# Performance work log

Measured on AMD Instinct MI355X. Metric: run time of the kernel, lower is better.

## Reference

```python
import jax, jax.numpy as jnp
import numpy as np

B, S, H, E, D = 4, 4096, 1024, 8, 256

def setup_inputs() -> dict:
    key = jax.random.key(0)
    k0, k1, k2, k3, k4 = jax.random.split(key, 5)
    scale_h = 1.0 / np.sqrt(H)
    scale_d = 1.0 / np.sqrt(D)
    return {
        "x": jax.random.normal(k0, (B, S, H), dtype=jnp.float32),
        "gate_w": jax.random.normal(k1, (E, H), dtype=jnp.float32) * scale_h,  # nn.Linear(H,E) weight [E,H]
        "wg": jax.random.normal(k2, (E, H, D), dtype=jnp.float32) * scale_h,   # gate_proj per expert
        "wu": jax.random.normal(k3, (E, H, D), dtype=jnp.float32) * scale_h,   # up_proj per expert
        "wd": jax.random.normal(k4, (E, D, H), dtype=jnp.float32) * scale_d,   # down_proj per expert
    }

def reference(x, gate_w, wg, wu, wd):
    b, s, h = x.shape
    xf = x.reshape(-1, h)                                   # [T, H]
    logits = jnp.einsum('th,eh->te', xf, gate_w)            # router logits
    expert_idx = jnp.argmax(logits, axis=-1)                # top-1 expert per token
    onehot = jax.nn.one_hot(expert_idx, gate_w.shape[0], dtype=x.dtype)  # [T, E]
    g = jnp.einsum('th,ehd->etd', xf, wg)                   # [E, T, D]
    u = jnp.einsum('th,ehd->etd', xf, wu)                   # [E, T, D]
    inter = jnp.square(jax.nn.relu(g)) * u                  # ReLU^2 * up
    inter = inter * onehot.T[:, :, None]                    # zero out non-selected (expert, token) pairs
    out = jnp.einsum('etd,edh->th', inter, wd)              # combine over experts
    return out.reshape(b, s, h)
```

## Files before the change

### kernel.cpp

```cpp
#include <hip/hip_runtime.h>
#include <hip/hip_bf16.h>

#define TOK 16384
#define HD  1024
#define DD  256
#define NE  8

typedef __attribute__((ext_vector_type(8))) short short8;
typedef __attribute__((ext_vector_type(4))) float floatx4;
typedef unsigned short u16;

static __device__ __forceinline__ u16 f2bf(float f) {
  __hip_bfloat16 h = __float2bfloat16(f);
  return *reinterpret_cast<u16*>(&h);
}
static __device__ __forceinline__ short8 cvt8(const float* p) {
  float4 a = *(const float4*)p;
  float4 b = *(const float4*)(p + 4);
  u16 t[8] = {f2bf(a.x), f2bf(a.y), f2bf(a.z), f2bf(a.w),
              f2bf(b.x), f2bf(b.y), f2bf(b.z), f2bf(b.w)};
  return *(short8*)t;
}

__global__ __launch_bounds__(256) void prep_kernel(
    const float* __restrict__ wg, const float* __restrict__ wu,
    const float* __restrict__ wd, const float* __restrict__ x,
    const float* __restrict__ gw,
    u16* __restrict__ wgT, u16* __restrict__ wuT, u16* __restrict__ wdT,
    u16* __restrict__ xbf,
    int* __restrict__ counts, int* __restrict__ tlist)
{
  __shared__ u16 tile[64][72];
  __shared__ int sexp[16];
  __shared__ int sbase[NE];
  int bid = blockIdx.x;
  int tid = threadIdx.x;

  if (bid < 1536) {
    const float* src; u16* dst; int R, C;
    if (bid < 512)       { src = wg; dst = wgT; R = HD; C = DD; }
    else if (bid < 1024) { src = wu; dst = wuT; R = HD; C = DD; bid -= 512; }
    else                 { src = wd; dst = wdT; R = DD; C = HD; bid -= 1024; }
    int e = bid >> 6, t = bid & 63;
    int ntc = C >> 6;
    int tr = t / ntc, tc = t % ntc;
    int r = tid >> 2, c0 = (tid & 3) * 16;
    const float* s = src + (size_t)e * R * C + (size_t)(tr * 64 + r) * C + tc * 64 + c0;
    *(short8*)&tile[r][c0]     = cvt8(s);
    *(short8*)&tile[r][c0 + 8] = cvt8(s + 8);
    __syncthreads();
    int c = tid >> 2, r0 = (tid & 3) * 16;
    alignas(16) u16 buf[16];
    for (int j = 0; j < 16; ++j) buf[j] = tile[r0 + j][c];
    u16* d = dst + (size_t)e * R * C + (size_t)(tc * 64 + c) * R + tr * 64 + r0;
    *(float4*)(d)     = *(const float4*)&buf[0];
    *(float4*)(d + 8) = *(const float4*)&buf[8];
    return;
  }

  int lane = tid & 63, wave = tid >> 6;
  int tok0 = (bid - 1536) * 16;
  for (int i = 0; i < 4; ++i) {
    int li = wave * 4 + i;
    int t = tok0 + li;
    const float* xp = x + (size_t)t * HD + lane * 16;
    float4 x0 = *(const float4*)xp,       x1 = *(const float4*)(xp + 4);
    float4 x2 = *(const float4*)(xp + 8), x3 = *(const float4*)(xp + 12);
    {
      alignas(16) u16 b[16] = {
        f2bf(x0.x), f2bf(x0.y), f2bf(x0.z), f2bf(x0.w),
        f2bf(x1.x), f2bf(x1.y), f2bf(x1.z), f2bf(x1.w),
        f2bf(x2.x), f2bf(x2.y), f2bf(x2.z), f2bf(x2.w),
        f2bf(x3.x), f2bf(x3.y), f2bf(x3.z), f2bf(x3.w)};
      u16* xd = xbf + (size_t)t * HD + lane * 16;
      *(float4*)xd       = *(const float4*)&b[0];
      *(float4*)(xd + 8) = *(const float4*)&b[8];
    }
    float acc[NE];
    for (int e = 0; e < NE; ++e) {
      const float* gp = gw + e * HD + lane * 16;
      float4 g0 = *(const float4*)gp,       g1 = *(const float4*)(gp + 4);
      float4 g2 = *(const float4*)(gp + 8), g3 = *(const float4*)(gp + 12);
      acc[e] = x0.x*g0.x + x0.y*g0.y + x0.z*g0.z + x0.w*g0.w
             + x1.x*g1.x + x1.y*g1.y + x1.z*g1.z + x1.w*g1.w
             + x2.x*g2.x + x2.y*g2.y + x2.z*g2.z + x2.w*g2.w
             + x3.x*g3.x + x3.y*g3.y + x3.z*g3.z + x3.w*g3.w;
    }
    for (int off = 32; off >= 1; off >>= 1)
      for (int e = 0; e < NE; ++e) acc[e] += __shfl_xor(acc[e], off, 64);
    if (lane == 0) {
      int be = 0; float bv = acc[0];
      for (int e = 1; e < NE; ++e) if (acc[e] > bv) { bv = acc[e]; be = e; }
      sexp[li] = be;
    }
  }
  __syncthreads();
  if (tid < NE) {
    int c = 0;
    for (int i = 0; i < 16; ++i) c += (sexp[i] == tid) ? 1 : 0;
    sbase[tid] = c ? atomicAdd(&counts[tid], c) : 0;
  }
  __syncthreads();
  if (tid < 16) {
    int e = sexp[tid], rank = 0;
    for (int i = 0; i < tid; ++i) rank += (sexp[i] == e) ? 1 : 0;
    tlist[e * TOK + sbase[e] + rank] = tok0 + tid;
  }
}

__global__ __launch_bounds__(256) void gemm1_kernel(
    const u16* __restrict__ xbf, const u16* __restrict__ wgT,
    const u16* __restrict__ wuT,
    const int* __restrict__ counts, const int* __restrict__ tlist,
    u16* __restrict__ inter)
{
  int bid = blockIdx.x;
  int e = bid & 7, half = (bid >> 3) & 1, tile = bid >> 4;
  int cnt = counts[e];
  int row0 = tile * 64;
  if (row0 >= cnt) return;

  __shared__ int stok[64];
  __shared__ u16 xA[64][40];
  __shared__ u16 sB[256][40];

  int tid = threadIdx.x, lane = tid & 63, wave = tid >> 6;
  if (tid < 64) {
    int r = row0 + tid;
    stok[tid] = tlist[e * TOK + (r < cnt ? r : cnt - 1)];
  }
  __syncthreads();
  int rmax = cnt - row0; if (rmax > 64) rmax = 64;

  int col = lane & 15, quad = lane >> 4;
  int at = tid >> 2, ac = (tid & 3) * 8;
  const u16* axp = xbf + (size_t)stok[at] * HD + ac;

  const u16* bp[4];
  for (int i = 0; i < 4; ++i) {
    int id = i * 256 + tid;
    int n = id >> 2, c = (id & 3) * 8;
    const u16* base = (n < 128) ? (wgT + ((size_t)e * DD + half * 128 + n) * HD)
                                : (wuT + ((size_t)e * DD + half * 128 + (n - 128)) * HD);
    bp[i] = base + c;
  }

  floatx4 acc[4][4];
  floatx4 zz = {0.f, 0.f, 0.f, 0.f};
  for (int m = 0; m < 4; ++m) for (int j = 0; j < 4; ++j) acc[m][j] = zz;

  for (int k0 = 0; k0 < HD; k0 += 32) {
    short8 av = *(const short8*)(axp + k0);
    short8 bv[4];
    for (int i = 0; i < 4; ++i) bv[i] = *(const short8*)(bp[i] + k0);
    __syncthreads();
    *(short8*)&xA[at][ac] = av;
    for (int i = 0; i < 4; ++i) {
      int id = i * 256 + tid;
      *(short8*)&sB[id >> 2][(id & 3) * 8] = bv[i];
    }
    __syncthreads();
    short8 af[4], bfr[4];
    for (int m = 0; m < 4; ++m) af[m] = *(const short8*)&xA[m * 16 + col][quad * 8];
    bfr[0] = *(const short8*)&sB[wave * 32 + col][quad * 8];
    bfr[1] = *(const short8*)&sB[wave * 32 + 16 + col][quad * 8];
    bfr[2] = *(const short8*)&sB[128 + wave * 32 + col][quad * 8];
    bfr[3] = *(const short8*)&sB[128 + wave * 32 + 16 + col][quad * 8];
    for (int m = 0; m < 4; ++m)
      for (int j = 0; j < 4; ++j)
        acc[m][j] = __builtin_amdgcn_mfma_f32_16x16x32_bf16(af[m], bfr[j], acc[m][j], 0, 0, 0);
  }

  for (int m = 0; m < 4; ++m)
    for (int jj = 0; jj < 2; ++jj)
      for (int r = 0; r < 4; ++r) {
        int row = m * 16 + quad * 4 + r;
        if (row < rmax) {
          float g = acc[m][jj][r]; g = g > 0.f ? g : 0.f;
          float u = acc[m][jj + 2][r];
          inter[(size_t)stok[row] * DD + half * 128 + wave * 32 + jj * 16 + col] = f2bf(g * g * u);
        }
      }
}

__global__ __launch_bounds__(256) void gemm2_kernel(
    const u16* __restrict__ inter, const u16* __restrict__ wdT,
    const int* __restrict__ counts, const int* __restrict__ tlist,
    float* __restrict__ out)
{
  int bid = blockIdx.x;
  int e = bid & 7, q = (bid >> 3) & 3, tile = bid >> 5;
  int cnt = counts[e];
  int row0 = tile * 64;
  if (row0 >= cnt) return;
  int n0 = q * 256;

  __shared__ int stok[64];
  __shared__ u16 sA[64][40];
  __shared__ __align__(16) u16 sBraw[256 * 40];
  u16 (*sB)[40] = (u16(*)[40])sBraw;
  float (*st)[260] = (float(*)[260])sBraw;

  int tid = threadIdx.x, lane = tid & 63, wave = tid >> 6;
  if (tid < 64) {
    int r = row0 + tid;
    stok[tid] = tlist[e * TOK + (r < cnt ? r : cnt - 1)];
  }
  __syncthreads();
  int rmax = cnt - row0; if (rmax > 64) rmax = 64;

  int col = lane & 15, quad = lane >> 4;
  int at = tid >> 2, ac = (tid & 3) * 8;
  const u16* aip = inter + (size_t)stok[at] * DD + ac;

  floatx4 acc[4][4];
  floatx4 zz = {0.f, 0.f, 0.f, 0.f};
  for (int m = 0; m < 4; ++m) for (int j = 0; j < 4; ++j) acc[m][j] = zz;

  for (int k0 = 0; k0 < DD; k0 += 32) {
    short8 av = *(const short8*)(aip + k0);
    short8 bv[4];
    for (int i = 0; i < 4; ++i) {
      int id = i * 256 + tid;
      int n = id >> 2, c = (id & 3) * 8;
      bv[i] = *(const short8*)(wdT + ((size_t)e * HD + n0 + n) * DD + k0 + c);
    }
    __syncthreads();
    *(short8*)&sA[at][ac] = av;
    for (int i = 0; i < 4; ++i) {
      int id = i * 256 + tid;
      *(short8*)&sB[id >> 2][(id & 3) * 8] = bv[i];
    }
    __syncthreads();
    short8 af[4], bfr[4];
    for (int m = 0; m < 4; ++m) af[m] = *(const short8*)&sA[m * 16 + col][quad * 8];
    for (int j = 0; j < 4; ++j) bfr[j] = *(const short8*)&sB[wave * 64 + j * 16 + col][quad * 8];
    for (int m = 0; m < 4; ++m)
      for (int j = 0; j < 4; ++j)
        acc[m][j] = __builtin_amdgcn_mfma_f32_16x16x32_bf16(af[m], bfr[j], acc[m][j], 0, 0, 0);
  }

  for (int m = 0; m < 4; ++m) {
    __syncthreads();
    for (int j = 0; j < 4; ++j)
      for (int r = 0; r < 4; ++r)
        st[quad * 4 + r][wave * 64 + j * 16 + col] = acc[m][j][r];
    __syncthreads();
    for (int i = 0; i < 4; ++i) {
      int id = i * 256 + tid;
      int r = id >> 6, c4 = (id & 63) * 4;
      int row = m * 16 + r;
      if (row < rmax)
        *(float4*)(out + (size_t)stok[row] * HD + n0 + c4) = *(const float4*)&st[r][c4];
    }
  }
}

extern "C" void kernel_launch(void* const* d_in, const int* in_sizes, int n_in,
                              void* d_out, int out_size, void* d_ws, size_t ws_size,
                              hipStream_t stream) {
  const float* x  = (const float*)d_in[0];
  const float* gw = (const float*)d_in[1];
  const float* wg = (const float*)d_in[2];
  const float* wu = (const float*)d_in[3];
  const float* wd = (const float*)d_in[4];
  float* out = (float*)d_out;

  char* ws = (char*)d_ws;
  int* counts = (int*)ws;
  int* tlist  = (int*)(ws + 256);
  u16* wgT   = (u16*)(ws + 524544);
  u16* wuT   = wgT + (size_t)NE * DD * HD;
  u16* wdT   = wuT + (size_t)NE * DD * HD;
  u16* inter = wdT + (size_t)NE * HD * DD;
  u16* xbf   = (u16*)d_out;

  hipMemsetAsync(counts, 0, NE * sizeof(int), stream);
  prep_kernel<<<1536 + TOK / 16, 256, 0, stream>>>(wg, wu, wd, x, gw,
                                                   wgT, wuT, wdT, xbf, counts, tlist);
  gemm1_kernel<<<4096, 256, 0, stream>>>(xbf, wgT, wuT, counts, tlist, inter);
  gemm2_kernel<<<8192, 256, 0, stream>>>(inter, wdT, counts, tlist, out);
}
```

Before: 226.5 us.

## Drop LDS staging in MoE GEMMs for direct register loads with double-buffered prefetch

Both GEMM kernels stop staging A and B tiles through shared memory with two barriers per k-step. Each lane now loads its MFMA fragments straight from global memory into registers, and two register sets are double-buffered so the next loads overlap the current MFMAs. Launch bounds are raised to two blocks per CU. The router prep also batches four tokens per wave to amortise the gate-weight loads and the shuffle reductions. The cost is lost data reuse across waves: A rows are reloaded by all four waves, so global and L2 traffic rise, and register pressure grows.

```diff
diff --git a/kernel.cpp b/kernel.cpp
--- a/kernel.cpp
+++ b/kernel.cpp
@@ -20,6 +20,28 @@
   u16 t[8] = {f2bf(a.x), f2bf(a.y), f2bf(a.z), f2bf(a.w),
               f2bf(b.x), f2bf(b.y), f2bf(b.z), f2bf(b.w)};
   return *(short8*)t;
+}
+
+static __device__ __forceinline__ void load_set(
+    short8 (&Sa)[2][4], short8 (&Sb)[2][4],
+    const u16* const (&aB)[4], const u16* const (&bB)[4], int kk) {
+#pragma unroll
+  for (int h = 0; h < 2; ++h) {
+#pragma unroll
+    for (int m = 0; m < 4; ++m) Sa[h][m] = *(const short8*)(aB[m] + kk + h * 32);
+#pragma unroll
+    for (int j = 0; j < 4; ++j) Sb[h][j] = *(const short8*)(bB[j] + kk + h * 32);
+  }
+}
+static __device__ __forceinline__ void mfma_set(
+    floatx4 (&acc)[4][4], short8 (&Sa)[2][4], short8 (&Sb)[2][4]) {
+#pragma unroll
+  for (int h = 0; h < 2; ++h)
+#pragma unroll
+    for (int m = 0; m < 4; ++m)
+#pragma unroll
+      for (int j = 0; j < 4; ++j)
+        acc[m][j] = __builtin_amdgcn_mfma_f32_16x16x32_bf16(Sa[h][m], Sb[h][j], acc[m][j], 0, 0, 0);
 }
 
 __global__ __launch_bounds__(256) void prep_kernel(
@@ -59,39 +81,52 @@
   }
 
   int lane = tid & 63, wave = tid >> 6;
-  int tok0 = (bid - 1536) * 16;
-  for (int i = 0; i < 4; ++i) {
-    int li = wave * 4 + i;
-    int t = tok0 + li;
-    const float* xp = x + (size_t)t * HD + lane * 16;
-    float4 x0 = *(const float4*)xp,       x1 = *(const float4*)(xp + 4);
-    float4 x2 = *(const float4*)(xp + 8), x3 = *(const float4*)(xp + 12);
-    {
-      alignas(16) u16 b[16] = {
-        f2bf(x0.x), f2bf(x0.y), f2bf(x0.z), f2bf(x0.w),
-        f2bf(x1.x), f2bf(x1.y), f2bf(x1.z), f2bf(x1.w),
-        f2bf(x2.x), f2bf(x2.y), f2bf(x2.z), f2bf(x2.w),
-        f2bf(x3.x), f2bf(x3.y), f2bf(x3.z), f2bf(x3.w)};
-      u16* xd = xbf + (size_t)t * HD + lane * 16;
-      *(float4*)xd       = *(const float4*)&b[0];
-      *(float4*)(xd + 8) = *(const float4*)&b[8];
+  int tok0 = (bid - 1536) * 16 + wave * 4;
+  float4 xr[4][4];
+#pragma unroll
+  for (int t = 0; t < 4; ++t) {
+    const float* xp = x + (size_t)(tok0 + t) * HD + lane * 16;
+    xr[t][0] = *(const float4*)xp;
+    xr[t][1] = *(const float4*)(xp + 4);
+    xr[t][2] = *(const float4*)(xp + 8);
+    xr[t][3] = *(const float4*)(xp + 12);
+  }
+#pragma unroll
+  for (int t = 0; t < 4; ++t) {
+    alignas(16) u16 b[16] = {
+      f2bf(xr[t][0].x), f2bf(xr[t][0].y), f2bf(xr[t][0].z), f2bf(xr[t][0].w),
+      f2bf(xr[t][1].x), f2bf(xr[t][1].y), f2bf(xr[t][1].z), f2bf(xr[t][1].w),
+      f2bf(xr[t][2].x), f2bf(xr[t][2].y), f2bf(xr[t][2].z), f2bf(xr[t][2].w),
+      f2bf(xr[t][3].x), f2bf(xr[t][3].y), f2bf(xr[t][3].z), f2bf(xr[t][3].w)};
+    u16* xd = xbf + (size_t)(tok0 + t) * HD + lane * 16;
+    *(float4*)xd       = *(const float4*)&b[0];
+    *(float4*)(xd + 8) = *(const float4*)&b[8];
+  }
+  float acc[4][NE];
+#pragma unroll
+  for (int e = 0; e < NE; ++e) {
+    const float* gp = gw + e * HD + lane * 16;
+    float4 g0 = *(const float4*)gp,       g1 = *(const float4*)(gp + 4);
+    float4 g2 = *(const float4*)(gp + 8), g3 = *(const float4*)(gp + 12);
+#pragma unroll
+    for (int t = 0; t < 4; ++t) {
+      acc[t][e] = xr[t][0].x*g0.x + xr[t][0].y*g0.y + xr[t][0].z*g0.z + xr[t][0].w*g0.w
+                + xr[t][1].x*g1.x + xr[t][1].y*g1.y + xr[t][1].z*g1.z + xr[t][1].w*g1.w
+                + xr[t][2].x*g2.x + xr[t][2].y*g2.y + xr[t][2].z*g2.z + xr[t][2].w*g2.w
+                + xr[t][3].x*g3.x + xr[t][3].y*g3.y + xr[t][3].z*g3.z + xr[t][3].w*g3.w;
     }
-    float acc[NE];
-    for (int e = 0; e < NE; ++e) {
-      const float* gp = gw + e * HD + lane * 16;
-      float4 g0 = *(const float4*)gp,       g1 = *(const float4*)(gp + 4);
-      float4 g2 = *(const float4*)(gp + 8), g3 = *(const float4*)(gp + 12);
-      acc[e] = x0.x*g0.x + x0.y*g0.y + x0.z*g0.z + x0.w*g0.w
-             + x1.x*g1.x + x1.y*g1.y + x1.z*g1.z + x1.w*g1.w
-             + x2.x*g2.x + x2.y*g2.y + x2.z*g2.z + x2.w*g2.w
-             + x3.x*g3.x + x3.y*g3.y + x3.z*g3.z + x3.w*g3.w;
-    }
-    for (int off = 32; off >= 1; off >>= 1)
-      for (int e = 0; e < NE; ++e) acc[e] += __shfl_xor(acc[e], off, 64);
-    if (lane == 0) {
-      int be = 0; float bv = acc[0];
-      for (int e = 1; e < NE; ++e) if (acc[e] > bv) { bv = acc[e]; be = e; }
-      sexp[li] = be;
+  }
+  for (int off = 32; off >= 1; off >>= 1)
+#pragma unroll
+    for (int t = 0; t < 4; ++t)
+#pragma unroll
+      for (int e = 0; e < NE; ++e) acc[t][e] += __shfl_xor(acc[t][e], off, 64);
+  if (lane == 0) {
+#pragma unroll
+    for (int t = 0; t < 4; ++t) {
+      int be = 0; float bv = acc[t][0];
+      for (int e = 1; e < NE; ++e) if (acc[t][e] > bv) { bv = acc[t][e]; be = e; }
+      sexp[wave * 4 + t] = be;
     }
   }
   __syncthreads();
@@ -104,11 +139,11 @@
   if (tid < 16) {
     int e = sexp[tid], rank = 0;
     for (int i = 0; i < tid; ++i) rank += (sexp[i] == e) ? 1 : 0;
-    tlist[e * TOK + sbase[e] + rank] = tok0 + tid;
-  }
-}
-
-__global__ __launch_bounds__(256) void gemm1_kernel(
+    tlist[e * TOK + sbase[e] + rank] = (bid - 1536) * 16 + tid;
+  }
+}
+
+__global__ __launch_bounds__(256, 2) void gemm1_kernel(
     const u16* __restrict__ xbf, const u16* __restrict__ wgT,
     const u16* __restrict__ wuT,
     const int* __restrict__ counts, const int* __restrict__ tlist,
@@ -121,9 +156,6 @@
   if (row0 >= cnt) return;
 
   __shared__ int stok[64];
-  __shared__ u16 xA[64][40];
-  __shared__ u16 sB[256][40];
-
   int tid = threadIdx.x, lane = tid & 63, wave = tid >> 6;
   if (tid < 64) {
     int r = row0 + tid;
@@ -133,46 +165,40 @@
   int rmax = cnt - row0; if (rmax > 64) rmax = 64;
 
   int col = lane & 15, quad = lane >> 4;
-  int at = tid >> 2, ac = (tid & 3) * 8;
-  const u16* axp = xbf + (size_t)stok[at] * HD + ac;
-
-  const u16* bp[4];
-  for (int i = 0; i < 4; ++i) {
-    int id = i * 256 + tid;
-    int n = id >> 2, c = (id & 3) * 8;
-    const u16* base = (n < 128) ? (wgT + ((size_t)e * DD + half * 128 + n) * HD)
-                                : (wuT + ((size_t)e * DD + half * 128 + (n - 128)) * HD);
-    bp[i] = base + c;
-  }
+
+  const u16* aB[4];
+#pragma unroll
+  for (int m = 0; m < 4; ++m)
+    aB[m] = xbf + (size_t)stok[m * 16 + col] * HD + quad * 8;
+  int nb = e * DD + half * 128 + wave * 32 + col;
+  const u16* bB[4];
+  bB[0] = wgT + (size_t)nb * HD + quad * 8;
+  bB[1] = wgT + (size_t)(nb + 16) * HD + quad * 8;
+  bB[2] = wuT + (size_t)nb * HD + quad * 8;
+  bB[3] = wuT + (size_t)(nb + 16) * HD + quad * 8;
 
   floatx4 acc[4][4];
   floatx4 zz = {0.f, 0.f, 0.f, 0.f};
-  for (int m = 0; m < 4; ++m) for (int j = 0; j < 4; ++j) acc[m][j] = zz;
-
-  for (int k0 = 0; k0 < HD; k0 += 32) {
-    short8 av = *(const short8*)(axp + k0);
-    short8 bv[4];
-    for (int i = 0; i < 4; ++i) bv[i] = *(const short8*)(bp[i] + k0);
-    __syncthreads();
-    *(short8*)&xA[at][ac] = av;
-    for (int i = 0; i < 4; ++i) {
-      int id = i * 256 + tid;
-      *(short8*)&sB[id >> 2][(id & 3) * 8] = bv[i];
-    }
-    __syncthreads();
-    short8 af[4], bfr[4];
-    for (int m = 0; m < 4; ++m) af[m] = *(const short8*)&xA[m * 16 + col][quad * 8];
-    bfr[0] = *(const short8*)&sB[wave * 32 + col][quad * 8];
-    bfr[1] = *(const short8*)&sB[wave * 32 + 16 + col][quad * 8];
-    bfr[2] = *(const short8*)&sB[128 + wave * 32 + col][quad * 8];
-    bfr[3] = *(const short8*)&sB[128 + wave * 32 + 16 + col][quad * 8];
-    for (int m = 0; m < 4; ++m)
-      for (int j = 0; j < 4; ++j)
-        acc[m][j] = __builtin_amdgcn_mfma_f32_16x16x32_bf16(af[m], bfr[j], acc[m][j], 0, 0, 0);
-  }
-
-  for (int m = 0; m < 4; ++m)
+#pragma unroll
+  for (int m = 0; m < 4; ++m)
+#pragma unroll
+    for (int j = 0; j < 4; ++j) acc[m][j] = zz;
+
+  short8 Pa[2][4], Pb[2][4], Qa[2][4], Qb[2][4];
+  load_set(Pa, Pb, aB, bB, 0);
+  load_set(Qa, Qb, aB, bB, 64);
+  for (int k0 = 0; k0 < HD; k0 += 128) {
+    mfma_set(acc, Pa, Pb);
+    if (k0 + 128 < HD) load_set(Pa, Pb, aB, bB, k0 + 128);
+    mfma_set(acc, Qa, Qb);
+    if (k0 + 192 < HD) load_set(Qa, Qb, aB, bB, k0 + 192);
+  }
+
+#pragma unroll
+  for (int m = 0; m < 4; ++m)
+#pragma unroll
     for (int jj = 0; jj < 2; ++jj)
+#pragma unroll
       for (int r = 0; r < 4; ++r) {
         int row = m * 16 + quad * 4 + r;
         if (row < rmax) {
@@ -183,7 +209,7 @@
       }
 }
 
-__global__ __launch_bounds__(256) void gemm2_kernel(
+__global__ __launch_bounds__(256, 2) void gemm2_kernel(
     const u16* __restrict__ inter, const u16* __restrict__ wdT,
     const int* __restrict__ counts, const int* __restrict__ tlist,
     float* __restrict__ out)
@@ -196,10 +222,7 @@
   int n0 = q * 256;
 
   __shared__ int stok[64];
-  __shared__ u16 sA[64][40];
-  __shared__ __align__(16) u16 sBraw[256 * 40];
-  u16 (*sB)[40] = (u16(*)[40])sBraw;
-  float (*st)[260] = (float(*)[260])sBraw;
+  __shared__ float st[16][260];
 
   int tid = threadIdx.x, lane = tid & 63, wave = tid >> 6;
   if (tid < 64) {
@@ -210,42 +233,43 @@
   int rmax = cnt - row0; if (rmax > 64) rmax = 64;
 
   int col = lane & 15, quad = lane >> 4;
-  int at = tid >> 2, ac = (tid & 3) * 8;
-  const u16* aip = inter + (size_t)stok[at] * DD + ac;
+
+  const u16* aB[4];
+#pragma unroll
+  for (int m = 0; m < 4; ++m)
+    aB[m] = inter + (size_t)stok[m * 16 + col] * DD + quad * 8;
+  int nb = e * HD + n0 + wave * 64 + col;
+  const u16* bB[4];
+#pragma unroll
+  for (int j = 0; j < 4; ++j)
+    bB[j] = wdT + (size_t)(nb + j * 16) * DD + quad * 8;
 
   floatx4 acc[4][4];
   floatx4 zz = {0.f, 0.f, 0.f, 0.f};
-  for (int m = 0; m < 4; ++m) for (int j = 0; j < 4; ++j) acc[m][j] = zz;
-
-  for (int k0 = 0; k0 < DD; k0 += 32) {
-    short8 av = *(const short8*)(aip + k0);
-    short8 bv[4];
-    for (int i = 0; i < 4; ++i) {
-      int id = i * 256 + tid;
-      int n = id >> 2, c = (id & 3) * 8;
-      bv[i] = *(const short8*)(wdT + ((size_t)e * HD + n0 + n) * DD + k0 + c);
-    }
-    __syncthreads();
-    *(short8*)&sA[at][ac] = av;
-    for (int i = 0; i < 4; ++i) {
-      int id = i * 256 + tid;
-      *(short8*)&sB[id >> 2][(id & 3) * 8] = bv[i];
-    }
-    __syncthreads();
-    short8 af[4], bfr[4];
-    for (int m = 0; m < 4; ++m) af[m] = *(const short8*)&sA[m * 16 + col][quad * 8];
-    for (int j = 0; j < 4; ++j) bfr[j] = *(const short8*)&sB[wave * 64 + j * 16 + col][quad * 8];
-    for (int m = 0; m < 4; ++m)
-      for (int j = 0; j < 4; ++j)
-        acc[m][j] = __builtin_amdgcn_mfma_f32_16x16x32_bf16(af[m], bfr[j], acc[m][j], 0, 0, 0);
+#pragma unroll
+  for (int m = 0; m < 4; ++m)
+#pragma unroll
+    for (int j = 0; j < 4; ++j) acc[m][j] = zz;
+
+  short8 Pa[2][4], Pb[2][4], Qa[2][4], Qb[2][4];
+  load_set(Pa, Pb, aB, bB, 0);
+  load_set(Qa, Qb, aB, bB, 64);
+  for (int k0 = 0; k0 < DD; k0 += 128) {
+    mfma_set(acc, Pa, Pb);
+    if (k0 + 128 < DD) load_set(Pa, Pb, aB, bB, k0 + 128);
+    mfma_set(acc, Qa, Qb);
+    if (k0 + 192 < DD) load_set(Qa, Qb, aB, bB, k0 + 192);
   }
 
   for (int m = 0; m < 4; ++m) {
     __syncthreads();
+#pragma unroll
     for (int j = 0; j < 4; ++j)
+#pragma unroll
       for (int r = 0; r < 4; ++r)
         st[quad * 4 + r][wave * 64 + j * 16 + col] = acc[m][j][r];
     __syncthreads();
+#pragma unroll
     for (int i = 0; i < 4; ++i) {
       int id = i * 256 + tid;
       int r = id >> 6, c4 = (id & 63) * 4;
```

New measurement: 290.1 us. 1.28x slower.
